# Performance work log

Measured on AMD Instinct MI355X. Metric: run time of the kernel, lower is better.

## Reference

```python
import jax, jax.numpy as jnp
import numpy as np


def setup_inputs() -> dict:
    key = jax.random.key(0)
    k1, k2, k3 = jax.random.split(key, 3)
    B, N, C = 4, 1024, 768
    x = jax.random.normal(k1, (B, N, C), dtype=jnp.float32)
    w_qkv = jax.random.normal(k2, (C, 3 * C), dtype=jnp.float32) * 0.02
    b_qkv = jnp.zeros((3 * C,), dtype=jnp.float32)
    w_proj = jax.random.normal(k3, (C, C), dtype=jnp.float32) * 0.02
    b_proj = jnp.zeros((C,), dtype=jnp.float32)
    return {"x": x, "w_qkv": w_qkv, "b_qkv": b_qkv,
            "w_proj": w_proj, "b_proj": b_proj, "num_heads": 12}


def reference(x, w_qkv, b_qkv, w_proj, b_proj, num_heads):
    B, N, C = x.shape
    h = num_heads
    d = C // h
    qkv = x @ w_qkv + b_qkv                       # (B, N, 3C)
    # einops '(h d qkv)': qkv index is innermost -> reshape to (B,N,h,d,3)
    qkv = qkv.reshape(B, N, h, d, 3)
    qkv = jnp.transpose(qkv, (4, 0, 2, 1, 3))     # (3, B, h, N, d)
    q, k, v = qkv[0], qkv[1], qkv[2]
    scaling = jnp.sqrt(jnp.asarray(C, dtype=x.dtype))  # NOTE: sqrt(embed_size), per source
    attn = jnp.einsum('bhqd,bhkd->bhqk', q, k) / scaling
    attn = jax.nn.softmax(attn, axis=-1)
    out = jnp.einsum('bhqk,bhkd->bhqd', attn, v)  # (B, h, N, d)
    out = jnp.transpose(out, (0, 2, 1, 3)).reshape(B, N, C)
    return out @ w_proj + b_proj
```

## Files before the change

kernel.cpp:

```cpp
#include <hip/hip_runtime.h>
#include <cstdint>

typedef __attribute__((ext_vector_type(8))) short short8;
typedef __attribute__((ext_vector_type(4))) short short4v;
typedef __attribute__((ext_vector_type(4))) float f32x4;
typedef unsigned short ushort_t;

#define MFMA(a, b, c) __builtin_amdgcn_mfma_f32_16x16x32_bf16(a, b, c, 0, 0, 0)

__device__ __forceinline__ ushort_t f2bf(float f) {
    unsigned u = __float_as_uint(f);
    u += 0x7FFF + ((u >> 16) & 1);
    return (ushort_t)(u >> 16);
}

__device__ __forceinline__ void gld_lds16(const ushort_t* g, ushort_t* l) {
    __builtin_amdgcn_global_load_lds(
        (__attribute__((address_space(1))) void*)g,
        (__attribute__((address_space(3))) void*)l, 16, 0, 0);
}

__global__ __launch_bounds__(256) void prep(
    const float* __restrict__ x, ushort_t* __restrict__ x_bf,
    const float* __restrict__ w_qkv, ushort_t* __restrict__ wqT,
    const float* __restrict__ w_proj, ushort_t* __restrict__ wpT,
    const float* __restrict__ b_qkv, float* __restrict__ bq_p, float scale) {
    __shared__ float t[64][68];
    const int bid = blockIdx.x;
    const int tid = threadIdx.x;

    if (bid < 1536) {
        int i = (bid * 256 + tid) * 8;
        float4 a = *(const float4*)&x[i];
        float4 b = *(const float4*)&x[i + 4];
        uint4 v;
        v.x = f2bf(a.x) | (f2bf(a.y) << 16);
        v.y = f2bf(a.z) | (f2bf(a.w) << 16);
        v.z = f2bf(b.x) | (f2bf(b.y) << 16);
        v.w = f2bf(b.z) | (f2bf(b.w) << 16);
        *(uint4*)&x_bf[i] = v;
        return;
    }
    if (bid < 2112) {
        const int qkv_mode = bid < 1968;
        const int local = qkv_mode ? bid - 1536 : bid - 1968;
        const int nbx = qkv_mode ? 36 : 12;
        const int J = qkv_mode ? 2304 : 768;
        const float* w = qkv_mode ? w_qkv : w_proj;
        ushort_t* out = qkv_mode ? wqT : wpT;
        const int j0 = (local % nbx) * 64;
        const int k0 = (local / nbx) * 64;
        const int K = 768;
        for (int g = tid; g < 1024; g += 256) {
            int r = g >> 4, c4 = g & 15;
            float4 v = *(const float4*)&w[(size_t)(k0 + r) * J + j0 + c4 * 4];
            *(float4*)&t[r][c4 * 4] = v;
        }
        __syncthreads();
        const int jj = tid >> 2, kc = tid & 3;
        const int j = j0 + jj;
        int jp; float s;
        if (qkv_mode) {
            int which = j % 3, hh = j / 192, d = (j % 192) / 3;
            jp = which * 768 + hh * 64 + d;
            s = (which == 0) ? scale : 1.f;
        } else { jp = j; s = 1.f; }
        ushort_t o[16];
        #pragma unroll
        for (int i = 0; i < 16; ++i) o[i] = f2bf(t[kc * 16 + i][jj] * s);
        uint4 v0, v1;
        v0.x = o[0] | (o[1] << 16);  v0.y = o[2] | (o[3] << 16);
        v0.z = o[4] | (o[5] << 16);  v0.w = o[6] | (o[7] << 16);
        v1.x = o[8] | (o[9] << 16);  v1.y = o[10] | (o[11] << 16);
        v1.z = o[12] | (o[13] << 16); v1.w = o[14] | (o[15] << 16);
        *(uint4*)&out[(size_t)jp * K + k0 + kc * 16] = v0;
        *(uint4*)&out[(size_t)jp * K + k0 + kc * 16 + 8] = v1;
        return;
    }
    {
        int j = (bid - 2112) * 256 + tid;
        if (j < 2304) {
            int which = j % 3, hh = j / 192, d = (j % 192) / 3;
            bq_p[which * 768 + hh * 64 + d] = b_qkv[j] * (which == 0 ? scale : 1.f);
        }
    }
}

template <int MODE, int BN>
__global__ __launch_bounds__(256, 4) void gemm_mfma(
    const ushort_t* __restrict__ A, const ushort_t* __restrict__ Bt,
    const float* __restrict__ bias, void* __restrict__ Cout,
    ushort_t* __restrict__ Vt, int M, int N, int K) {
    constexpr int WC = BN / 64;
    constexpr int WR = 4 / WC;
    constexpr int MT = 128 / WR / 16;
    constexpr int AELEM = 128 * 32;
    constexpr int BELEM = BN * 32;

    __shared__ ushort_t As[2 * AELEM];
    __shared__ ushort_t Bs[2 * BELEM];

    const int tid = threadIdx.x;
    const int lane = tid & 63;
    const int wv = tid >> 6;
    const int wr = wv / WC, wc = wv % WC;
    const int l15 = lane & 15;
    const int lg = lane >> 4;

    const int m0 = blockIdx.y * 128;
    const int n0 = blockIdx.x * BN;

    const int rbase = tid >> 2;
    const int c4l = tid & 3;
    const int swz8 = (c4l ^ (rbase & 3)) * 8;

    const ushort_t* gA = A + (size_t)(m0 + rbase) * K + swz8;
    const ushort_t* gB = Bt + (size_t)(n0 + rbase) * K + swz8;

    auto stage = [&](int buf, int k0) {
        ushort_t* la = As + buf * AELEM + tid * 8;
        ushort_t* lb = Bs + buf * BELEM + tid * 8;
        #pragma unroll
        for (int rr = 0; rr < 2; ++rr)
            gld_lds16(gA + (size_t)rr * 64 * K + k0, la + rr * 2048);
        #pragma unroll
        for (int rr = 0; rr < BN / 64; ++rr)
            gld_lds16(gB + (size_t)rr * 64 * K + k0, lb + rr * 2048);
    };

    f32x4 acc[MT][4];
    #pragma unroll
    for (int i = 0; i < MT; ++i)
        #pragma unroll
        for (int j = 0; j < 4; ++j) acc[i][j] = (f32x4){0.f, 0.f, 0.f, 0.f};

    const int nk = K >> 5;
    stage(0, 0);
    __syncthreads();

    int cur = 0;
    for (int t = 0; t < nk; ++t) {
        if (t + 1 < nk) stage(cur ^ 1, (t + 1) * 32);
        const ushort_t* as = As + cur * AELEM;
        const ushort_t* bs = Bs + cur * BELEM;
        short8 af[MT], bfr[4];
        #pragma unroll
        for (int mt = 0; mt < MT; ++mt) {
            int row = wr * (16 * MT) + mt * 16 + l15;
            int gr = lg ^ (row & 3);
            af[mt] = *(const short8*)&as[row * 32 + gr * 8];
        }
        #pragma unroll
        for (int nt = 0; nt < 4; ++nt) {
            int row = wc * 64 + nt * 16 + l15;
            int gr = lg ^ (row & 3);
            bfr[nt] = *(const short8*)&bs[row * 32 + gr * 8];
        }
        #pragma unroll
        for (int mt = 0; mt < MT; ++mt)
            #pragma unroll
            for (int nt = 0; nt < 4; ++nt)
                acc[mt][nt] = MFMA(af[mt], bfr[nt], acc[mt][nt]);
        __syncthreads();
        cur ^= 1;
    }

    if (MODE == 1 && n0 >= 1536) {
        #pragma unroll
        for (int nt = 0; nt < 4; ++nt) {
            int col = n0 + wc * 64 + nt * 16 + l15;
            int dg = col - 1536;
            int hh = dg >> 6, dd = dg & 63;
            float bb = bias[col];
            #pragma unroll
            for (int mt = 0; mt < MT; ++mt) {
                int row0 = m0 + wr * (16 * MT) + mt * 16 + lg * 4;
                int bb_ = row0 >> 10, n = row0 & 1023;
                short4v pv = {(short)f2bf(acc[mt][nt][0] + bb),
                              (short)f2bf(acc[mt][nt][1] + bb),
                              (short)f2bf(acc[mt][nt][2] + bb),
                              (short)f2bf(acc[mt][nt][3] + bb)};
                *(short4v*)&Vt[(size_t)(bb_ * 12 + hh) * 65536 + (size_t)dd * 1024 + n] = pv;
            }
        }
        return;
    }

    #pragma unroll
    for (int nt = 0; nt < 4; ++nt) {
        int col = n0 + wc * 64 + nt * 16 + l15;
        float bb = bias[col];
        #pragma unroll
        for (int mt = 0; mt < MT; ++mt) {
            int row = m0 + wr * (16 * MT) + mt * 16 + lg * 4;
            #pragma unroll
            for (int r = 0; r < 4; ++r) {
                float v = acc[mt][nt][r] + bb;
                if (MODE == 1)
                    ((ushort_t*)Cout)[(size_t)(row + r) * N + col] = f2bf(v);
                else
                    ((float*)Cout)[(size_t)(row + r) * N + col] = v;
            }
        }
    }
}

__global__ __launch_bounds__(256, 3) void attn_mfma(
    const ushort_t* __restrict__ qkv,
    const ushort_t* __restrict__ Vt,
    ushort_t* __restrict__ outp) {
    __shared__ ushort_t Qs[4096];
    __shared__ ushort_t Ks[2 * 4096];
    __shared__ ushort_t Vs[2 * 4096];
    __shared__ ushort_t Ps[4096];

    const int tid = threadIdx.x;
    const int lane = tid & 63;
    const int wv = tid >> 6;
    const int l15 = lane & 15;
    const int lg = lane >> 4;

    const int bh = blockIdx.y;
    const int b = bh / 12, h = bh % 12;
    const int q0 = blockIdx.x * 64;

    const int rbase = tid >> 3;
    const int c8l = tid & 7;
    const int swz8 = (c8l ^ (rbase & 7)) * 8;

    const ushort_t* gQ = qkv + (size_t)(b * 1024 + q0 + rbase) * 2304 + h * 64 + swz8;
    const ushort_t* gK = qkv + (size_t)(b * 1024 + rbase) * 2304 + 768 + h * 64 + swz8;
    const ushort_t* gV = Vt + (size_t)bh * 65536 + (size_t)rbase * 1024 + swz8;

    auto stageKV = [&](int buf, int kt) {
        gld_lds16(gK + (size_t)(kt * 64) * 2304, Ks + buf * 4096 + tid * 8);
        gld_lds16(gK + (size_t)(kt * 64 + 32) * 2304, Ks + buf * 4096 + 2048 + tid * 8);
        gld_lds16(gV + kt * 64, Vs + buf * 4096 + tid * 8);
        gld_lds16(gV + kt * 64 + 32 * 1024, Vs + buf * 4096 + 2048 + tid * 8);
    };

    gld_lds16(gQ, Qs + tid * 8);
    gld_lds16(gQ + (size_t)32 * 2304, Qs + tid * 8 + 2048);
    stageKV(0, 0);
    __syncthreads();

    short8 bq[2];
    {
        int row = wv * 16 + l15;
        #pragma unroll
        for (int kk = 0; kk < 2; ++kk) {
            int gr = (kk * 4 + lg) ^ (row & 7);
            bq[kk] = *(const short8*)&Qs[row * 64 + gr * 8];
        }
    }

    float m_run = -1e30f, l_run = 0.f;
    f32x4 o[4];
    #pragma unroll
    for (int dt = 0; dt < 4; ++dt) o[dt] = (f32x4){0.f, 0.f, 0.f, 0.f};

    ushort_t* pb = Ps + wv * 1024;

    int cur = 0;
    for (int kt = 0; kt < 16; ++kt) {
        if (kt < 15) stageKV(cur ^ 1, kt + 1);
        const ushort_t* ks = Ks + cur * 4096;
        const ushort_t* vs = Vs + cur * 4096;

        f32x4 s[4];
        #pragma unroll
        for (int st = 0; st < 4; ++st) {
            int row = st * 16 + l15;
            short8 a0 = *(const short8*)&ks[row * 64 + (((0 + lg) ^ (row & 7)) * 8)];
            short8 a1 = *(const short8*)&ks[row * 64 + (((4 + lg) ^ (row & 7)) * 8)];
            f32x4 z = (f32x4){0.f, 0.f, 0.f, 0.f};
            z = MFMA(a0, bq[0], z);
            z = MFMA(a1, bq[1], z);
            s[st] = z;
        }

        float mloc = -1e30f;
        #pragma unroll
        for (int st = 0; st < 4; ++st)
            #pragma unroll
            for (int r = 0; r < 4; ++r) mloc = fmaxf(mloc, s[st][r]);
        mloc = fmaxf(mloc, __shfl_xor(mloc, 16));
        mloc = fmaxf(mloc, __shfl_xor(mloc, 32));

        float psum = 0.f;
        if (__all(mloc <= m_run + 8.f)) {
            #pragma unroll
            for (int st = 0; st < 4; ++st)
                #pragma unroll
                for (int r = 0; r < 4; ++r) {
                    float p = __builtin_amdgcn_exp2f(s[st][r] - m_run);
                    s[st][r] = p;
                    psum += p;
                }
            psum += __shfl_xor(psum, 16);
            psum += __shfl_xor(psum, 32);
            l_run += psum;
        } else {
            float mnew = fmaxf(m_run, mloc);
            float corr = __builtin_amdgcn_exp2f(m_run - mnew);
            #pragma unroll
            for (int st = 0; st < 4; ++st)
                #pragma unroll
                for (int r = 0; r < 4; ++r) {
                    float p = __builtin_amdgcn_exp2f(s[st][r] - mnew);
                    s[st][r] = p;
                    psum += p;
                }
            psum += __shfl_xor(psum, 16);
            psum += __shfl_xor(psum, 32);
            l_run = l_run * corr + psum;
            m_run = mnew;
            #pragma unroll
            for (int dt = 0; dt < 4; ++dt)
                #pragma unroll
                for (int r = 0; r < 4; ++r) o[dt][r] *= corr;
        }

        #pragma unroll
        for (int st = 0; st < 4; ++st) {
            int g8 = st * 2 + (lg >> 1);
            int byteoff = l15 * 128 + ((g8 ^ (l15 & 7)) * 16) + (lg & 1) * 8;
            short4v pv = {(short)f2bf(s[st][0]), (short)f2bf(s[st][1]),
                          (short)f2bf(s[st][2]), (short)f2bf(s[st][3])};
            *(short4v*)((char*)pb + byteoff) = pv;
        }

        #pragma unroll
        for (int kk = 0; kk < 2; ++kk) {
            int grp = (kk * 4 + lg) ^ (l15 & 7);
            short8 bp = *(const short8*)&pb[l15 * 64 + grp * 8];
            #pragma unroll
            for (int dt = 0; dt < 4; ++dt) {
                int row = dt * 16 + l15;
                int ga = (kk * 4 + lg) ^ (row & 7);
                short8 av = *(const short8*)&vs[row * 64 + ga * 8];
                o[dt] = MFMA(av, bp, o[dt]);
            }
        }
        __syncthreads();
        cur ^= 1;
    }

    const float inv = 1.f / l_run;
    #pragma unroll
    for (int dt = 0; dt < 4; ++dt) {
        short4v pv = {(short)f2bf(o[dt][0] * inv), (short)f2bf(o[dt][1] * inv),
                      (short)f2bf(o[dt][2] * inv), (short)f2bf(o[dt][3] * inv)};
        *(short4v*)&pb[l15 * 64 + dt * 16 + lg * 4] = pv;
    }
    #pragma unroll
    for (int pass = 0; pass < 2; ++pass) {
        int idx = pass * 64 + lane;
        int row = idx >> 3, c8 = idx & 7;
        uint4 v = *(const uint4*)&pb[row * 64 + c8 * 8];
        *(uint4*)&outp[(size_t)(b * 1024 + q0 + wv * 16 + row) * 768 + h * 64 + c8 * 8] = v;
    }
}

extern "C" void kernel_launch(void* const* d_in, const int* in_sizes, int n_in,
                              void* d_out, int out_size, void* d_ws, size_t ws_size,
                              hipStream_t stream) {
    const float* x = (const float*)d_in[0];
    const float* w_qkv = (const float*)d_in[1];
    const float* b_qkv = (const float*)d_in[2];
    const float* w_proj = (const float*)d_in[3];
    const float* b_proj = (const float*)d_in[4];
    float* outp = (float*)d_out;

    char* ws = (char*)d_ws;
    ushort_t* x_bf = (ushort_t*)ws;   ws += (size_t)4096 * 768 * 2;
    ushort_t* wqT = (ushort_t*)ws;    ws += (size_t)2304 * 768 * 2;
    ushort_t* wpT = (ushort_t*)ws;    ws += (size_t)768 * 768 * 2;
    float* bq_p = (float*)ws;         ws += (size_t)2304 * 4;
    ushort_t* qkv_bf = (ushort_t*)ws; ws += (size_t)4096 * 2304 * 2;
    ushort_t* Vt = (ushort_t*)ws;     ws += (size_t)48 * 64 * 1024 * 2;
    ushort_t* aout = (ushort_t*)ws;

    const float scale = 0.036084391824351615f * 1.4426950408889634f;

    prep<<<2121, 256, 0, stream>>>(x, x_bf, w_qkv, wqT, w_proj, wpT,
                                   b_qkv, bq_p, scale);

    gemm_mfma<1, 128><<<dim3(18, 32), 256, 0, stream>>>(
        x_bf, wqT, bq_p, qkv_bf, Vt, 4096, 2304, 768);

    attn_mfma<<<dim3(16, 48), 256, 0, stream>>>(qkv_bf, Vt, aout);

    gemm_mfma<0, 64><<<dim3(12, 32), 256, 0, stream>>>(
        aout, wpT, b_proj, outp, nullptr, 4096, 768, 768);
}
```

Before: 85.61 us.

## Restructure GEMM to two waves per block with larger per-wave tiles

The GEMM kernel now runs 128 threads (two wavefronts) instead of 256, and each wave computes a 64-row by full-BN tile (MT=4, NT=BN/16), so per-wave fragment reuse goes up. Staging loops and the LDS swizzle are adjusted to match the new thread count, and the swizzle now keys on row pairs. The aim is fewer LDS fragment loads per MFMA and less block overhead. In exchange there are more accumulator registers per thread (up to 32 f32x4 for BN=128), fewer waves per block to hide latency, and occupancy bounds loosen to 2.

```diff
diff --git a/kernel.cpp b/kernel.cpp
--- a/kernel.cpp
+++ b/kernel.cpp
@@ -87,13 +87,12 @@
 }
 
 template <int MODE, int BN>
-__global__ __launch_bounds__(256, 4) void gemm_mfma(
+__global__ __launch_bounds__(128, 2) void gemm_mfma(
     const ushort_t* __restrict__ A, const ushort_t* __restrict__ Bt,
     const float* __restrict__ bias, void* __restrict__ Cout,
     ushort_t* __restrict__ Vt, int M, int N, int K) {
-    constexpr int WC = BN / 64;
-    constexpr int WR = 4 / WC;
-    constexpr int MT = 128 / WR / 16;
+    constexpr int MT = 4;
+    constexpr int NT = BN / 16;
     constexpr int AELEM = 128 * 32;
     constexpr int BELEM = BN * 32;
 
@@ -103,7 +102,6 @@
     const int tid = threadIdx.x;
     const int lane = tid & 63;
     const int wv = tid >> 6;
-    const int wr = wv / WC, wc = wv % WC;
     const int l15 = lane & 15;
     const int lg = lane >> 4;
 
@@ -112,7 +110,7 @@
 
     const int rbase = tid >> 2;
     const int c4l = tid & 3;
-    const int swz8 = (c4l ^ (rbase & 3)) * 8;
+    const int swz8 = (c4l ^ ((rbase >> 1) & 3)) * 8;
 
     const ushort_t* gA = A + (size_t)(m0 + rbase) * K + swz8;
     const ushort_t* gB = Bt + (size_t)(n0 + rbase) * K + swz8;
@@ -121,18 +119,18 @@
         ushort_t* la = As + buf * AELEM + tid * 8;
         ushort_t* lb = Bs + buf * BELEM + tid * 8;
         #pragma unroll
-        for (int rr = 0; rr < 2; ++rr)
-            gld_lds16(gA + (size_t)rr * 64 * K + k0, la + rr * 2048);
-        #pragma unroll
-        for (int rr = 0; rr < BN / 64; ++rr)
-            gld_lds16(gB + (size_t)rr * 64 * K + k0, lb + rr * 2048);
+        for (int rr = 0; rr < 4; ++rr)
+            gld_lds16(gA + (size_t)rr * 32 * K + k0, la + rr * 1024);
+        #pragma unroll
+        for (int rr = 0; rr < BN / 32; ++rr)
+            gld_lds16(gB + (size_t)rr * 32 * K + k0, lb + rr * 1024);
     };
 
-    f32x4 acc[MT][4];
+    f32x4 acc[MT][NT];
     #pragma unroll
     for (int i = 0; i < MT; ++i)
         #pragma unroll
-        for (int j = 0; j < 4; ++j) acc[i][j] = (f32x4){0.f, 0.f, 0.f, 0.f};
+        for (int j = 0; j < NT; ++j) acc[i][j] = (f32x4){0.f, 0.f, 0.f, 0.f};
 
     const int nk = K >> 5;
     stage(0, 0);
@@ -143,23 +141,23 @@
         if (t + 1 < nk) stage(cur ^ 1, (t + 1) * 32);
         const ushort_t* as = As + cur * AELEM;
         const ushort_t* bs = Bs + cur * BELEM;
-        short8 af[MT], bfr[4];
+        short8 af[MT], bfr[NT];
         #pragma unroll
         for (int mt = 0; mt < MT; ++mt) {
-            int row = wr * (16 * MT) + mt * 16 + l15;
-            int gr = lg ^ (row & 3);
+            int row = wv * 64 + mt * 16 + l15;
+            int gr = lg ^ ((row >> 1) & 3);
             af[mt] = *(const short8*)&as[row * 32 + gr * 8];
         }
         #pragma unroll
-        for (int nt = 0; nt < 4; ++nt) {
-            int row = wc * 64 + nt * 16 + l15;
-            int gr = lg ^ (row & 3);
+        for (int nt = 0; nt < NT; ++nt) {
+            int row = nt * 16 + l15;
+            int gr = lg ^ ((row >> 1) & 3);
             bfr[nt] = *(const short8*)&bs[row * 32 + gr * 8];
         }
         #pragma unroll
         for (int mt = 0; mt < MT; ++mt)
             #pragma unroll
-            for (int nt = 0; nt < 4; ++nt)
+            for (int nt = 0; nt < NT; ++nt)
                 acc[mt][nt] = MFMA(af[mt], bfr[nt], acc[mt][nt]);
         __syncthreads();
         cur ^= 1;
@@ -167,14 +165,14 @@
 
     if (MODE == 1 && n0 >= 1536) {
         #pragma unroll
-        for (int nt = 0; nt < 4; ++nt) {
-            int col = n0 + wc * 64 + nt * 16 + l15;
+        for (int nt = 0; nt < NT; ++nt) {
+            int col = n0 + nt * 16 + l15;
             int dg = col - 1536;
             int hh = dg >> 6, dd = dg & 63;
             float bb = bias[col];
             #pragma unroll
             for (int mt = 0; mt < MT; ++mt) {
-                int row0 = m0 + wr * (16 * MT) + mt * 16 + lg * 4;
+                int row0 = m0 + wv * 64 + mt * 16 + lg * 4;
                 int bb_ = row0 >> 10, n = row0 & 1023;
                 short4v pv = {(short)f2bf(acc[mt][nt][0] + bb),
                               (short)f2bf(acc[mt][nt][1] + bb),
@@ -187,12 +185,12 @@
     }
 
     #pragma unroll
-    for (int nt = 0; nt < 4; ++nt) {
-        int col = n0 + wc * 64 + nt * 16 + l15;
+    for (int nt = 0; nt < NT; ++nt) {
+        int col = n0 + nt * 16 + l15;
         float bb = bias[col];
         #pragma unroll
         for (int mt = 0; mt < MT; ++mt) {
-            int row = m0 + wr * (16 * MT) + mt * 16 + lg * 4;
+            int row = m0 + wv * 64 + mt * 16 + lg * 4;
             #pragma unroll
             for (int r = 0; r < 4; ++r) {
                 float v = acc[mt][nt][r] + bb;
@@ -386,11 +384,11 @@
     prep<<<2121, 256, 0, stream>>>(x, x_bf, w_qkv, wqT, w_proj, wpT,
                                    b_qkv, bq_p, scale);
 
-    gemm_mfma<1, 128><<<dim3(18, 32), 256, 0, stream>>>(
+    gemm_mfma<1, 128><<<dim3(18, 32), 128, 0, stream>>>(
         x_bf, wqT, bq_p, qkv_bf, Vt, 4096, 2304, 768);
 
     attn_mfma<<<dim3(16, 48), 256, 0, stream>>>(qkv_bf, Vt, aout);
 
-    gemm_mfma<0, 64><<<dim3(12, 32), 256, 0, stream>>>(
+    gemm_mfma<0, 64><<<dim3(12, 32), 128, 0, stream>>>(
         aout, wpT, b_proj, outp, nullptr, 4096, 768, 768);
 }
```

After: 90.74 us. 6.0% more time.
